# Kernel tuning notes

Hardware: AMD Instinct MI355X
Metric: run time of the kernel (lower is better)

The kernel has to match this reference:

```python
import jax, jax.numpy as jnp
import numpy as np

N, IN_DIM, OUT_DIM, HEADS, SUB = 4096, 256, 128, 4, 32
ETA = 0.5
LAMBDA_SPARSE = 0.05
NEG_BIG = -1e9


def setup_inputs() -> dict:
    key = jax.random.key(0)
    k1, k2, k3, k4 = jax.random.split(key, 4)
    H = jax.random.normal(k1, (N, IN_DIM), dtype=jnp.float32)
    # sparse binary adjacency mask (avg degree ~ 41) with self-loops
    adj_mask = (jax.random.uniform(k2, (N, N)) < 0.01).astype(jnp.float32)
    adj_mask = adj_mask.at[jnp.arange(N), jnp.arange(N)].set(1.0)
    # per-head orthonormal subspace bases U_k = QR(randn)[:, :SUB]
    raw = jax.random.normal(k3, (HEADS, IN_DIM, SUB), dtype=jnp.float32)
    U = jax.vmap(lambda r: jnp.linalg.qr(r)[0])(raw)  # [h, D, s]
    threshold = jnp.full((OUT_DIM,), LAMBDA_SPARSE, dtype=jnp.float32)
    proj_w = jax.random.normal(k4, (OUT_DIM, IN_DIM), dtype=jnp.float32) / np.float32(np.sqrt(IN_DIM))
    return {"H": H, "adj_mask": adj_mask, "U": U, "threshold": threshold, "proj_w": proj_w}


def reference(H, adj_mask, U, threshold, proj_w):
    # Z_k = U_k^T @ H^T  -> [h, s, N]
    Z = jnp.einsum('hds,nd->hsn', U, H)
    # scores_k = Z_k^T @ Z_k / sqrt(s)  -> [h, N, N]
    scores = jnp.einsum('hsn,hsm->hnm', Z, Z) / jnp.sqrt(jnp.float32(SUB))
    scores = scores + (1.0 - adj_mask)[None, :, :] * NEG_BIG
    alpha = jax.nn.softmax(scores, axis=-1)  # torch softmax(dim=1) on [N,N] rows
    # agg_k = Z_k @ alpha_k^T  -> [h, s, N];  sum_k U_k @ agg_k -> [D, N]
    agg = jnp.einsum('hsj,hij->hsi', Z, alpha)
    agg_sum = jnp.einsum('hds,hsn->dn', U, agg)
    H_half = H + ETA * agg_sum.T           # [N, D]
    H_half = H_half @ proj_w.T             # [N, out_dim]
    # soft-threshold
    H_out = jnp.sign(H_half) * jax.nn.relu(jnp.abs(H_half) - threshold[None, :])
    # orthogonality loss: sum_k ||U_k^T U_k - I||_F^2 + sum_{k<l} ||U_k^T U_l||_F^2
    G = jnp.einsum('kds,ldt->klst', U, U)  # [h, h, s, s]
    eye_s = jnp.eye(SUB, dtype=U.dtype)
    eye_h = jnp.eye(HEADS, dtype=U.dtype)
    sub = G - eye_h[:, :, None, None] * eye_s[None, None, :, :]
    sq = jnp.sum(sub ** 2, axis=(2, 3))    # [h, h]
    orth_loss = jnp.sum(jnp.triu(jnp.ones((HEADS, HEADS), dtype=U.dtype)) * sq)
    return H_out, orth_loss
```

## Files before the change

### kernel.cpp

```cpp
#include <hip/hip_runtime.h>
#include <hip/hip_bf16.h>
#include <math.h>

#define NN 4096
#define IN_DIM 256
#define OUT_DIM 128
#define HEADS 4
#define SUB 32
#define MAXDEG 128
#define ETA 0.5f
#define INV_SQRT_SUB 0.17677669529663687f

typedef __attribute__((ext_vector_type(8))) short bf16x8;
typedef __attribute__((ext_vector_type(4))) short s16x4;
typedef __attribute__((ext_vector_type(4))) float f32x4;

static __device__ inline short f2bf(float f) {
    unsigned u = __float_as_uint(f);
    unsigned r = u + 0x7FFFu + ((u >> 16) & 1u);
    return (short)(r >> 16);
}
static __device__ inline float bf2f(short s) {
    return __uint_as_float(((unsigned)(unsigned short)s) << 16);
}
#define MFMA16(a, b, c) __builtin_amdgcn_mfma_f32_16x16x32_bf16(a, b, c, 0, 0, 0)

__global__ __launch_bounds__(256) void fused_small(const float* __restrict__ U,
                                                   const float* __restrict__ PW,
                                                   short* __restrict__ Wh,
                                                   short* __restrict__ Wl,
                                                   float* __restrict__ W2,
                                                   float* __restrict__ loss_parts) {
    int b = blockIdx.x;
    int t = threadIdx.x;
    __shared__ float sh[260];

    if (b < 256) {
        float v;
        if (b < 128) {
            int h = b >> 5, s = b & 31;
            v = U[h * IN_DIM * SUB + t * SUB + s];
        } else {
            v = PW[(b - 128) * IN_DIM + t];
        }
        short hi = f2bf(v);
        Wh[b * IN_DIM + t] = hi;
        Wl[b * IN_DIM + t] = f2bf(v - bf2f(hi));
    } else if (b < 384) {
        int hs = b - 256;
        int h = hs >> 5, s = hs & 31;
        sh[t] = U[h * IN_DIM * SUB + t * SUB + s];
        __syncthreads();
        if (t < 128) {
            const float4* pw4 = (const float4*)(PW + t * IN_DIM);
            const float4* u4  = (const float4*)sh;
            float acc = 0.f;
            #pragma unroll 4
            for (int d4 = 0; d4 < 64; ++d4) {
                float4 a = u4[d4], p = pw4[d4];
                acc += a.x * p.x + a.y * p.y + a.z * p.z + a.w * p.w;
            }
            W2[hs * OUT_DIM + t] = acc;
        }
    } else {
        const int pk[10] = {0,0,0,0,1,1,1,2,2,3};
        const int pl[10] = {0,1,2,3,1,2,3,2,3,3};
        int p = b - 384;
        int k = pk[p], l = pl[p];
        int t2 = t & 31;
        int sg = t >> 5;
        const float* Uk = U + k * IN_DIM * SUB;
        const float* Ul = U + l * IN_DIM * SUB;
        float a0 = 0.f, a1 = 0.f, a2 = 0.f, a3 = 0.f;
        #pragma unroll 4
        for (int d = 0; d < IN_DIM; ++d) {
            float ul = Ul[d * SUB + t2];
            float u0 = Uk[d * SUB + sg * 4 + 0];
            float u1 = Uk[d * SUB + sg * 4 + 1];
            float u2 = Uk[d * SUB + sg * 4 + 2];
            float u3 = Uk[d * SUB + sg * 4 + 3];
            a0 += u0 * ul; a1 += u1 * ul; a2 += u2 * ul; a3 += u3 * ul;
        }
        if (k == l) {
            if (sg * 4 + 0 == t2) a0 -= 1.f;
            if (sg * 4 + 1 == t2) a1 -= 1.f;
            if (sg * 4 + 2 == t2) a2 -= 1.f;
            if (sg * 4 + 3 == t2) a3 -= 1.f;
        }
        float local = a0 * a0 + a1 * a1 + a2 * a2 + a3 * a3;
        local += __shfl_xor(local, 32, 64);
        local += __shfl_xor(local, 16, 64);
        local += __shfl_xor(local, 8, 64);
        local += __shfl_xor(local, 4, 64);
        local += __shfl_xor(local, 2, 64);
        local += __shfl_xor(local, 1, 64);
        if ((t & 63) == 0) sh[256 + (t >> 6)] = local;
        __syncthreads();
        if (t == 0) loss_parts[p] = sh[256] + sh[257] + sh[258] + sh[259];
    }
}

#define LDA 264
__global__ __launch_bounds__(256) void ztp_mfma(const float* __restrict__ H,
                                                const short* __restrict__ Wh,
                                                const short* __restrict__ Wl,
                                                float* __restrict__ ZT,
                                                float* __restrict__ P) {
    __shared__ short Ah[16 * LDA];
    __shared__ short Al[16 * LDA];
    int t = threadIdx.x, b = blockIdx.x;
    int m0 = (b >> 1) * 16, chalf = b & 1;

    {
        int r = t >> 4, dbase = (t & 15) * 16;
        const float4* src = (const float4*)(H + (size_t)(m0 + r) * IN_DIM + dbase);
        #pragma unroll
        for (int q = 0; q < 4; ++q) {
            float4 f = src[q];
            float fv[4] = {f.x, f.y, f.z, f.w};
            s16x4 hi, lo;
            #pragma unroll
            for (int j = 0; j < 4; ++j) {
                short h = f2bf(fv[j]);
                hi[j] = h;
                lo[j] = f2bf(fv[j] - bf2f(h));
            }
            *(s16x4*)&Ah[r * LDA + dbase + q * 4] = hi;
            *(s16x4*)&Al[r * LDA + dbase + q * 4] = lo;
        }
    }
    __syncthreads();

    int wave = t >> 6, lane = t & 63;
    int c0 = chalf * 128 + wave * 32;
    int arow = lane & 15, agrp = lane >> 4;

    const short* ahp = &Ah[arow * LDA + agrp * 8];
    const short* alp = &Al[arow * LDA + agrp * 8];
    const short* bh0 = Wh + (size_t)(c0 + arow) * IN_DIM + agrp * 8;
    const short* bl0 = Wl + (size_t)(c0 + arow) * IN_DIM + agrp * 8;
    const short* bh1 = bh0 + 16 * IN_DIM;
    const short* bl1 = bl0 + 16 * IN_DIM;

    f32x4 acc0 = {0.f, 0.f, 0.f, 0.f};
    f32x4 acc1 = {0.f, 0.f, 0.f, 0.f};

    #pragma unroll
    for (int kk = 0; kk < 8; ++kk) {
        int d0 = kk * 32;
        bf16x8 a_h = *(const bf16x8*)(ahp + d0);
        bf16x8 a_l = *(const bf16x8*)(alp + d0);
        bf16x8 b0h = *(const bf16x8*)(bh0 + d0);
        bf16x8 b0l = *(const bf16x8*)(bl0 + d0);
        bf16x8 b1h = *(const bf16x8*)(bh1 + d0);
        bf16x8 b1l = *(const bf16x8*)(bl1 + d0);
        acc0 = MFMA16(a_h, b0h, acc0);
        acc0 = MFMA16(a_h, b0l, acc0);
        acc0 = MFMA16(a_l, b0h, acc0);
        acc1 = MFMA16(a_h, b1h, acc1);
        acc1 = MFMA16(a_h, b1l, acc1);
        acc1 = MFMA16(a_l, b1h, acc1);
    }

    float* dst = chalf ? P : ZT;
    int colbase = c0 - chalf * 128;
    #pragma unroll
    for (int i = 0; i < 4; ++i) {
        int row = m0 + agrp * 4 + i;
        dst[(size_t)row * 128 + colbase + arow]      = acc0[i];
        dst[(size_t)row * 128 + colbase + 16 + arow] = acc1[i];
    }
}

__global__ __launch_bounds__(128) void attn_core(const float* __restrict__ ZT,
                                                 const float* __restrict__ Pm,
                                                 const float* __restrict__ W2,
                                                 const float* __restrict__ adj,
                                                 const float* __restrict__ threshold,
                                                 const float* __restrict__ loss_parts,
                                                 float* __restrict__ out) {
    int i = blockIdx.x;
    int t = threadIdx.x;
    __shared__ int   nbr_s[MAXDEG];
    __shared__ float e_s[MAXDEG][HEADS];
    __shared__ float z_s[128];
    __shared__ float agg_s[128];
    __shared__ int cnt;

    if (i == 0 && t == 0) {
        float L = 0.f;
        #pragma unroll
        for (int p = 0; p < 10; ++p) L += loss_parts[p];
        out[(size_t)NN * OUT_DIM] = L;
    }

    const float4* row4 = (const float4*)(adj + (size_t)i * NN);
    float4 v[8];
    #pragma unroll
    for (int k = 0; k < 8; ++k) v[k] = row4[t + k * 128];

    if (t == 0) cnt = 0;
    nbr_s[t] = 0;
    z_s[t] = ZT[(size_t)i * 128 + t];
    __syncthreads();

    #pragma unroll
    for (int k = 0; k < 8; ++k) {
        int j0 = (t + k * 128) * 4;
        if (v[k].x > 0.5f) { int p = atomicAdd(&cnt, 1); if (p < MAXDEG) nbr_s[p] = j0; }
        if (v[k].y > 0.5f) { int p = atomicAdd(&cnt, 1); if (p < MAXDEG) nbr_s[p] = j0 + 1; }
        if (v[k].z > 0.5f) { int p = atomicAdd(&cnt, 1); if (p < MAXDEG) nbr_s[p] = j0 + 2; }
        if (v[k].w > 0.5f) { int p = atomicAdd(&cnt, 1); if (p < MAXDEG) nbr_s[p] = j0 + 3; }
    }
    __syncthreads();
    int dg = cnt < MAXDEG ? cnt : MAXDEG;

    int jj0 = t >> 2, h = t & 3;
    int ntiles = (dg + 31) >> 5;
    const float4* qr = (const float4*)(&z_s[h * 32]);
    for (int tile = 0; tile < ntiles; ++tile) {
        int jj = tile * 32 + jj0;
        int j = nbr_s[jj];
        const float4* zr = (const float4*)(ZT + (size_t)j * 128 + h * 32);
        float acc = 0.f;
        #pragma unroll
        for (int k = 0; k < 8; ++k) {
            float4 z = zr[k];
            float4 q = qr[k];
            acc += z.x * q.x + z.y * q.y + z.z * q.z + z.w * q.w;
        }
        e_s[jj][h] = (jj < dg) ? __expf(acc * INV_SQRT_SUB) : 0.f;
    }
    __syncthreads();

    int hh = t >> 5;
    float accV = 0.f, accS = 0.f;
    const float* zbase = ZT + t;
    for (int jj = 0; jj < dg; jj += 4) {
        int ja = nbr_s[jj],     jb = nbr_s[jj + 1];
        int jc = nbr_s[jj + 2], jd = nbr_s[jj + 3];
        float ea = e_s[jj][hh],     eb = e_s[jj + 1][hh];
        float ec = e_s[jj + 2][hh], ed = e_s[jj + 3][hh];
        float va = zbase[(size_t)ja * 128], vb = zbase[(size_t)jb * 128];
        float vc = zbase[(size_t)jc * 128], vd = zbase[(size_t)jd * 128];
        accV += ea * va + eb * vb + ec * vc + ed * vd;
        accS += (ea + eb) + (ec + ed);
    }
    agg_s[t] = accV * (ETA / accS);
    __syncthreads();

    float val = Pm[(size_t)i * 128 + t];
    #pragma unroll 4
    for (int q4 = 0; q4 < 32; ++q4) {
        int hs = q4 * 4;
        float w0 = W2[(hs + 0) * 128 + t];
        float w1 = W2[(hs + 1) * 128 + t];
        float w2v = W2[(hs + 2) * 128 + t];
        float w3 = W2[(hs + 3) * 128 + t];
        float4 a = *(const float4*)&agg_s[hs];
        val += a.x * w0 + a.y * w1 + a.z * w2v + a.w * w3;
    }
    float th = threshold[t];
    float av = fabsf(val) - th;
    out[(size_t)i * 128 + t] = (av > 0.f) ? copysignf(av, val) : 0.f;
}

extern "C" void kernel_launch(void* const* d_in, const int* in_sizes, int n_in,
                              void* d_out, int out_size, void* d_ws, size_t ws_size,
                              hipStream_t stream) {
    const float* H   = (const float*)d_in[0];
    const float* adj = (const float*)d_in[1];
    const float* U   = (const float*)d_in[2];
    const float* thr = (const float*)d_in[3];
    const float* PW  = (const float*)d_in[4];
    float* out = (float*)d_out;

    char* ws = (char*)d_ws;
    float* ZT    = (float*)(ws);
    float* P     = (float*)(ws + (size_t)2097152);
    float* W2    = (float*)(ws + (size_t)4194304);
    short* Wh    = (short*)(ws + (size_t)4259840);
    short* Wl    = (short*)(ws + (size_t)4390912);
    float* lossp = (float*)(ws + (size_t)4521984);

    fused_small<<<394, 256, 0, stream>>>(U, PW, Wh, Wl, W2, lossp);
    ztp_mfma<<<NN / 16 * 2, 256, 0, stream>>>(H, Wh, Wl, ZT, P);
    attn_core<<<NN, 128, 0, stream>>>(ZT, P, W2, adj, thr, lossp, out);
}
```

Measured before the change: 149.0 us.

## Move adjacency neighbor extraction into the first kernel and unroll gather loop

The dense adjacency scan that builds each row's neighbor list now runs as extra blocks of the first small kernel. Those blocks write compacted neighbor indices and degrees to workspace, and the attention kernel reads them instead of scanning a 4096-wide row. The aim is to take the 64MB adjacency read off the attention kernel's critical path so it overlaps with the small preprocessing work. The aggregation loop is also unrolled to 8 neighbors so more gathers are in flight, and the P and threshold loads are hoisted. The trade-off is an extra global write and read of the neighbor lists, and the 8-wide unroll relies on the lists being zero-padded past the degree.

```diff
diff --git a/kernel.cpp b/kernel.cpp
--- a/kernel.cpp
+++ b/kernel.cpp
@@ -27,13 +27,17 @@
 
 __global__ __launch_bounds__(256) void fused_small(const float* __restrict__ U,
                                                    const float* __restrict__ PW,
+                                                   const float* __restrict__ adj,
                                                    short* __restrict__ Wh,
                                                    short* __restrict__ Wl,
                                                    float* __restrict__ W2,
-                                                   float* __restrict__ loss_parts) {
+                                                   float* __restrict__ loss_parts,
+                                                   int* __restrict__ nbr,
+                                                   int* __restrict__ deg) {
     int b = blockIdx.x;
     int t = threadIdx.x;
     __shared__ float sh[260];
+    __shared__ int cnt2[2];
 
     if (b < 256) {
         float v;
@@ -62,7 +66,7 @@
             }
             W2[hs * OUT_DIM + t] = acc;
         }
-    } else {
+    } else if (b < 394) {
         const int pk[10] = {0,0,0,0,1,1,1,2,2,3};
         const int pl[10] = {0,1,2,3,1,2,3,2,3,3};
         int p = b - 384;
@@ -97,6 +101,29 @@
         if ((t & 63) == 0) sh[256 + (t >> 6)] = local;
         __syncthreads();
         if (t == 0) loss_parts[p] = sh[256] + sh[257] + sh[258] + sh[259];
+    } else {
+        int sb = b - 394;
+        int half = t >> 7, u = t & 127;
+        int row = sb * 2 + half;
+        const float4* row4 = (const float4*)(adj + (size_t)row * NN);
+        float4 v[8];
+        #pragma unroll
+        for (int k = 0; k < 8; ++k) v[k] = row4[u + k * 128];
+        if (u == 0) cnt2[half] = 0;
+        __syncthreads();
+        int* nrow = nbr + row * MAXDEG;
+        #pragma unroll
+        for (int k = 0; k < 8; ++k) {
+            int j0 = (u + k * 128) * 4;
+            if (v[k].x > 0.5f) { int p = atomicAdd(&cnt2[half], 1); if (p < MAXDEG) nrow[p] = j0; }
+            if (v[k].y > 0.5f) { int p = atomicAdd(&cnt2[half], 1); if (p < MAXDEG) nrow[p] = j0 + 1; }
+            if (v[k].z > 0.5f) { int p = atomicAdd(&cnt2[half], 1); if (p < MAXDEG) nrow[p] = j0 + 2; }
+            if (v[k].w > 0.5f) { int p = atomicAdd(&cnt2[half], 1); if (p < MAXDEG) nrow[p] = j0 + 3; }
+        }
+        __syncthreads();
+        int dgr = cnt2[half] < MAXDEG ? cnt2[half] : MAXDEG;
+        if (u >= dgr) nrow[u] = 0;
+        if (u == 0) deg[row] = dgr;
     }
 }
 
@@ -175,7 +202,8 @@
 __global__ __launch_bounds__(128) void attn_core(const float* __restrict__ ZT,
                                                  const float* __restrict__ Pm,
                                                  const float* __restrict__ W2,
-                                                 const float* __restrict__ adj,
+                                                 const int* __restrict__ nbr,
+                                                 const int* __restrict__ deg,
                                                  const float* __restrict__ threshold,
                                                  const float* __restrict__ loss_parts,
                                                  float* __restrict__ out) {
@@ -185,7 +213,6 @@
     __shared__ float e_s[MAXDEG][HEADS];
     __shared__ float z_s[128];
     __shared__ float agg_s[128];
-    __shared__ int cnt;
 
     if (i == 0 && t == 0) {
         float L = 0.f;
@@ -194,26 +221,15 @@
         out[(size_t)NN * OUT_DIM] = L;
     }
 
-    const float4* row4 = (const float4*)(adj + (size_t)i * NN);
-    float4 v[8];
-    #pragma unroll
-    for (int k = 0; k < 8; ++k) v[k] = row4[t + k * 128];
-
-    if (t == 0) cnt = 0;
-    nbr_s[t] = 0;
-    z_s[t] = ZT[(size_t)i * 128 + t];
+    int dg = deg[i];
+    int nb = nbr[i * MAXDEG + t];
+    float zq = ZT[(size_t)i * 128 + t];
+    float pval = Pm[(size_t)i * 128 + t];
+    float th = threshold[t];
+
+    nbr_s[t] = nb;
+    z_s[t] = zq;
     __syncthreads();
-
-    #pragma unroll
-    for (int k = 0; k < 8; ++k) {
-        int j0 = (t + k * 128) * 4;
-        if (v[k].x > 0.5f) { int p = atomicAdd(&cnt, 1); if (p < MAXDEG) nbr_s[p] = j0; }
-        if (v[k].y > 0.5f) { int p = atomicAdd(&cnt, 1); if (p < MAXDEG) nbr_s[p] = j0 + 1; }
-        if (v[k].z > 0.5f) { int p = atomicAdd(&cnt, 1); if (p < MAXDEG) nbr_s[p] = j0 + 2; }
-        if (v[k].w > 0.5f) { int p = atomicAdd(&cnt, 1); if (p < MAXDEG) nbr_s[p] = j0 + 3; }
-    }
-    __syncthreads();
-    int dg = cnt < MAXDEG ? cnt : MAXDEG;
 
     int jj0 = t >> 2, h = t & 3;
     int ntiles = (dg + 31) >> 5;
@@ -236,20 +252,27 @@
     int hh = t >> 5;
     float accV = 0.f, accS = 0.f;
     const float* zbase = ZT + t;
-    for (int jj = 0; jj < dg; jj += 4) {
-        int ja = nbr_s[jj],     jb = nbr_s[jj + 1];
-        int jc = nbr_s[jj + 2], jd = nbr_s[jj + 3];
-        float ea = e_s[jj][hh],     eb = e_s[jj + 1][hh];
-        float ec = e_s[jj + 2][hh], ed = e_s[jj + 3][hh];
-        float va = zbase[(size_t)ja * 128], vb = zbase[(size_t)jb * 128];
-        float vc = zbase[(size_t)jc * 128], vd = zbase[(size_t)jd * 128];
-        accV += ea * va + eb * vb + ec * vc + ed * vd;
-        accS += (ea + eb) + (ec + ed);
+    for (int jj = 0; jj < dg; jj += 8) {
+        int j0 = nbr_s[jj],     j1 = nbr_s[jj + 1];
+        int j2 = nbr_s[jj + 2], j3 = nbr_s[jj + 3];
+        int j4 = nbr_s[jj + 4], j5 = nbr_s[jj + 5];
+        int j6 = nbr_s[jj + 6], j7 = nbr_s[jj + 7];
+        float v0 = zbase[(size_t)j0 * 128], v1 = zbase[(size_t)j1 * 128];
+        float v2 = zbase[(size_t)j2 * 128], v3 = zbase[(size_t)j3 * 128];
+        float v4 = zbase[(size_t)j4 * 128], v5 = zbase[(size_t)j5 * 128];
+        float v6 = zbase[(size_t)j6 * 128], v7 = zbase[(size_t)j7 * 128];
+        float e0 = e_s[jj][hh],     e1 = e_s[jj + 1][hh];
+        float e2 = e_s[jj + 2][hh], e3 = e_s[jj + 3][hh];
+        float e4 = e_s[jj + 4][hh], e5 = e_s[jj + 5][hh];
+        float e6 = e_s[jj + 6][hh], e7 = e_s[jj + 7][hh];
+        accV += e0 * v0 + e1 * v1 + e2 * v2 + e3 * v3
+              + e4 * v4 + e5 * v5 + e6 * v6 + e7 * v7;
+        accS += (e0 + e1) + (e2 + e3) + (e4 + e5) + (e6 + e7);
     }
     agg_s[t] = accV * (ETA / accS);
     __syncthreads();
 
-    float val = Pm[(size_t)i * 128 + t];
+    float val = pval;
     #pragma unroll 4
     for (int q4 = 0; q4 < 32; ++q4) {
         int hs = q4 * 4;
@@ -260,7 +283,6 @@
         float4 a = *(const float4*)&agg_s[hs];
         val += a.x * w0 + a.y * w1 + a.z * w2v + a.w * w3;
     }
-    float th = threshold[t];
     float av = fabsf(val) - th;
     out[(size_t)i * 128 + t] = (av > 0.f) ? copysignf(av, val) : 0.f;
 }
@@ -282,8 +304,10 @@
     short* Wh    = (short*)(ws + (size_t)4259840);
     short* Wl    = (short*)(ws + (size_t)4390912);
     float* lossp = (float*)(ws + (size_t)4521984);
-
-    fused_small<<<394, 256, 0, stream>>>(U, PW, Wh, Wl, W2, lossp);
+    int*   nbr   = (int*)  (ws + (size_t)4530176);
+    int*   deg   = (int*)  (ws + (size_t)6627328);
+
+    fused_small<<<394 + NN / 2, 256, 0, stream>>>(U, PW, adj, Wh, Wl, W2, lossp, nbr, deg);
     ztp_mfma<<<NN / 16 * 2, 256, 0, stream>>>(H, Wh, Wl, ZT, P);
-    attn_core<<<NN, 128, 0, stream>>>(ZT, P, W2, adj, thr, lossp, out);
-}
+    attn_core<<<NN, 128, 0, stream>>>(ZT, P, W2, nbr, deg, thr, lossp, out);
+}
```

After: 154.3 us. +3.6%, slower.
